# Performance work log

Measured on AMD Instinct MI355X. Metric: run time of the kernel, lower is better.

The kernel has to match this reference:

```python
import jax, jax.numpy as jnp
import numpy as np

C = 256
B, H, W = 2, 64, 64


def conv1x1(x, Wt, b):
    # x: [B, Cin, H, W], Wt: [Cout, Cin], b: [Cout]
    return jnp.einsum('bchw,oc->bohw', x, Wt) + b[None, :, None, None]


def setup_inputs() -> dict:
    key = jax.random.key(0)
    ks = jax.random.split(key, 16)
    s = 0.02
    d = {
        'input1': jax.random.normal(ks[0], (B, C, H, W), jnp.float32),
        'input2': jax.random.normal(ks[1], (B, C, H, W), jnp.float32),
        'Wq1': jax.random.normal(ks[2], (C // 4, C), jnp.float32) * s,
        'bq1': jnp.zeros((C // 4,), jnp.float32),
        'Wk1': jax.random.normal(ks[3], (C // 2, C), jnp.float32) * s,
        'bk1': jnp.zeros((C // 2,), jnp.float32),
        'Wv1': jax.random.normal(ks[4], (C, C), jnp.float32) * s,
        'bv1': jnp.zeros((C,), jnp.float32),
        'Wq2': jax.random.normal(ks[5], (C // 4, C), jnp.float32) * s,
        'bq2': jnp.zeros((C // 4,), jnp.float32),
        'Wk2': jax.random.normal(ks[6], (C // 2, C), jnp.float32) * s,
        'bk2': jnp.zeros((C // 2,), jnp.float32),
        'Wv2': jax.random.normal(ks[7], (C, C), jnp.float32) * s,
        'bv2': jnp.zeros((C,), jnp.float32),
        'gamma': jax.random.normal(ks[8], (1,), jnp.float32) * 0.1,
    }
    return d


def reference(input1, input2, Wq1, bq1, Wk1, bk1, Wv1, bv1,
              Wq2, bq2, Wk2, bk2, Wv2, bv2, gamma):
    b, c, h, w = input1.shape
    hw = h * w
    q1 = conv1x1(input1, Wq1, bq1)                      # [B, C/4, H, W]
    k1 = conv1x1(input1, Wk1, bk1).reshape(b, -1, hw)   # [B, C/2, HW]
    v1 = conv1x1(input1, Wv1, bv1).reshape(b, -1, hw)   # [B, C,   HW]
    q2 = conv1x1(input2, Wq2, bq2)
    k2 = conv1x1(input2, Wk2, bk2).reshape(b, -1, hw)
    v2 = conv1x1(input2, Wv2, bv2).reshape(b, -1, hw)

    # cat on new dim 2 then 'b c t h w -> b (c t) h w' interleaves q1/q2 channels
    q = jnp.stack([q1, q2], axis=2).reshape(b, c // 2, hw)  # [B, C/2, HW]
    q = q.transpose(0, 2, 1)                                # [B, HW, C/2]

    a1 = jax.nn.softmax(jnp.einsum('bnc,bcm->bnm', q, k1), axis=-1)  # [B, HW, HW]
    out1 = jnp.einsum('bcm,bnm->bcn', v1, a1).reshape(b, c, h, w)
    out1 = gamma[0] * out1 + input1

    a2 = jax.nn.softmax(jnp.einsum('bnc,bcm->bnm', q, k2), axis=-1)
    out2 = jnp.einsum('bcm,bnm->bcn', v2, a2).reshape(b, c, h, w)
    out2 = gamma[0] * out2 + input2
    return (out1, out2)
```

## Files before the change

kernel.cpp:

```cpp
#include <hip/hip_runtime.h>

typedef __attribute__((ext_vector_type(8)))  short bf16x8;
typedef __attribute__((ext_vector_type(4)))  float f32x4;
typedef __attribute__((ext_vector_type(16))) float f32x16;
typedef __attribute__((ext_vector_type(8)))  unsigned short u16x8;

#define HW 4096
#define CDIM 256

#if __has_builtin(__builtin_amdgcn_exp2f)
#define EXP2(x) __builtin_amdgcn_exp2f(x)
#else
#define EXP2(x) exp2f(x)
#endif

__device__ __forceinline__ unsigned short f2bf(float f) {
    union { float f; unsigned u; } v; v.f = f;
    unsigned r = v.u + 0x7fffu + ((v.u >> 16) & 1u);
    return (unsigned short)(r >> 16);
}
__device__ __forceinline__ float bf2f(unsigned short u) {
    union { unsigned u; float f; } v; v.u = ((unsigned)u) << 16;
    return v.f;
}
__device__ __forceinline__ unsigned pk2(float hi, float lo) {
    union { float f; unsigned u; } a, b; a.f = hi; b.f = lo;
    return __builtin_amdgcn_perm(a.u, b.u, 0x07060302u);
}
__device__ __forceinline__ void gl_lds16(const void* g, void* l) {
    __builtin_amdgcn_global_load_lds(
        (const __attribute__((address_space(1))) unsigned int*)(unsigned long long)g,
        (__attribute__((address_space(3))) unsigned int*)(unsigned int)(unsigned long long)l,
        16, 0, 0);
}

__global__ __launch_bounds__(256) void wpack_kernel(
    const float* __restrict__ Wq1, const float* __restrict__ Wk1,
    const float* __restrict__ Wv1, const float* __restrict__ Wq2,
    const float* __restrict__ Wk2, const float* __restrict__ Wv2,
    unsigned short* __restrict__ Wpk)
{
    const int i  = blockIdx.x * 256 + threadIdx.x;
    const int c4 = i & 63;
    const int r6 = i >> 6;
    const int inp = r6 / 448;
    const int o   = r6 - inp * 448;
    const float* src;
    int orow;
    if (o < 64)       { src = inp ? Wq2 : Wq1; orow = o; }
    else if (o < 192) { src = inp ? Wk2 : Wk1; orow = o - 64; }
    else              { src = inp ? Wv2 : Wv1; orow = o - 192; }
    const float4 v = *(const float4*)(src + (size_t)orow * CDIM + c4 * 4);
    uint2 pkd; pkd.x = pk2(v.y, v.x); pkd.y = pk2(v.w, v.z);
    ((uint2*)Wpk)[i] = pkd;
}

__global__ __launch_bounds__(256) void proj_kernel(
    const float* __restrict__ in1, const float* __restrict__ in2,
    const float* __restrict__ bq1, const float* __restrict__ bk1,
    const float* __restrict__ bv1, const float* __restrict__ bq2,
    const float* __restrict__ bk2, const float* __restrict__ bv2,
    const unsigned short* __restrict__ Wpk,
    unsigned short* __restrict__ Qg, unsigned short* __restrict__ Kg,
    unsigned short* __restrict__ Vg)
{
    __shared__ unsigned xb[32 * 128];

    const int bid   = blockIdx.x;
    const int ntile = bid & 127;
    const int inp   = (bid >> 7) & 1;
    const int b     = bid >> 8;

    const float* X  = (inp ? in2 : in1) + (size_t)b * CDIM * HW;
    const float* bq = inp ? bq2 : bq1;
    const float* bk = inp ? bk2 : bk1;
    const float* bv = inp ? bv2 : bv1;
    const unsigned short* Wb = Wpk + (size_t)inp * 448 * CDIM;

    const int tid  = threadIdx.x;
    const int lane = tid & 63;
    const int w    = tid >> 6;
    const int l15  = lane & 15, quad = lane >> 4;
    const int n0   = ntile * 32;

#pragma unroll
    for (int t = 0; t < 4; ++t) {
        const int idx = t * 256 + tid;
        const int cp  = idx >> 3;
        const int n4  = idx & 7;
        const float* p0 = X + (size_t)(cp * 2) * HW + n0 + n4 * 4;
        const float4 a = *(const float4*)p0;
        const float4 bb = *(const float4*)(p0 + HW);
        const float av[4] = {a.x, a.y, a.z, a.w};
        const float bv4[4] = {bb.x, bb.y, bb.z, bb.w};
#pragma unroll
        for (int r = 0; r < 4; ++r) {
            const int n = n4 * 4 + r;
            xb[n * 128 + (((cp >> 2) ^ (n & 7)) << 2) + (cp & 3)] = pk2(bv4[r], av[r]);
        }
    }
    __syncthreads();

    f32x4 acc[7][2];
#pragma unroll
    for (int i = 0; i < 7; ++i)
#pragma unroll
        for (int j = 0; j < 2; ++j) acc[i][j] = (f32x4){0.f, 0.f, 0.f, 0.f};

#pragma unroll
    for (int kk = 0; kk < 8; ++kk) {
        bf16x8 xf[2];
#pragma unroll
        for (int ns = 0; ns < 2; ++ns) {
            const int nrow = ns * 16 + l15;
            xf[ns] = *(const bf16x8*)&xb[nrow * 128 + (((kk * 4 + quad) ^ (nrow & 7)) << 2)];
        }
#pragma unroll
        for (int os = 0; os < 7; ++os) {
            const int ob = w * 7 + os;
            const int og = ob * 16 + l15;
            const bf16x8 wf = *(const bf16x8*)(Wb + (size_t)og * CDIM + kk * 32 + quad * 8);
            if (ob < 12) {
#pragma unroll
                for (int ns = 0; ns < 2; ++ns)
                    acc[os][ns] = __builtin_amdgcn_mfma_f32_16x16x32_bf16(xf[ns], wf, acc[os][ns], 0, 0, 0);
            } else {
#pragma unroll
                for (int ns = 0; ns < 2; ++ns)
                    acc[os][ns] = __builtin_amdgcn_mfma_f32_16x16x32_bf16(wf, xf[ns], acc[os][ns], 0, 0, 0);
            }
        }
    }

    const size_t qbase = (size_t)b * HW * 128;
    const size_t kbase = (size_t)(b * 2 + inp) * HW * 128;
    const size_t vbase = (size_t)(b * 2 + inp) * (size_t)CDIM * HW;
#pragma unroll
    for (int os = 0; os < 7; ++os) {
        const int ob = w * 7 + os;
        if (ob < 4) {
            const int o = ob * 16 + l15;
            const float bb = bq[o];
#pragma unroll
            for (int ns = 0; ns < 2; ++ns) {
                const f32x4 d = acc[os][ns];
#pragma unroll
                for (int r = 0; r < 4; ++r) {
                    const int n = n0 + ns * 16 + quad * 4 + r;
                    Qg[qbase + (size_t)n * 128 + 2 * o + inp] =
                        f2bf((d[r] + bb) * 1.4426950408889634f);
                }
            }
        } else if (ob < 12) {
            const int c = (ob - 4) * 16 + l15;
            const float bb = bk[c];
#pragma unroll
            for (int ns = 0; ns < 2; ++ns) {
                const f32x4 d = acc[os][ns];
#pragma unroll
                for (int r = 0; r < 4; ++r) {
                    const int n = n0 + ns * 16 + quad * 4 + r;
                    Kg[kbase + (size_t)n * 128 + c] = f2bf(d[r] + bb);
                }
            }
        } else {
            const int c0 = (ob - 12) * 16 + quad * 4;
#pragma unroll
            for (int ns = 0; ns < 2; ++ns) {
                const f32x4 d = acc[os][ns];
#pragma unroll
                for (int r = 0; r < 4; ++r) {
                    const int n = n0 + ns * 16 + l15;
                    Vg[vbase + (size_t)(c0 + r) * HW + n] = f2bf(d[r] + bv[c0 + r]);
                }
            }
        }
    }
}

__global__ __launch_bounds__(256, 2) void attn_kernel(
    const unsigned short* __restrict__ Qg, const unsigned short* __restrict__ Kg,
    const unsigned short* __restrict__ Vg,
    unsigned short* __restrict__ Op, float* __restrict__ Lp)
{
    __shared__ unsigned short kbuf[2][32 * 16 * 8];
    __shared__ unsigned short vbuf[3][256 * 4 * 8];

    const int bid = blockIdx.x;
    const int mq  = bid & 3;
    const int set = (bid >> 2) & 3;
    const int att = set & 1, b = set >> 1;
    const int nt  = bid >> 4;
    const int n0g = nt * 128;
    const int mbase = mq * 1024;
    const int tid = threadIdx.x;
    const int lane = tid & 63, w = tid >> 6;
    const int l31 = lane & 31, h = lane >> 5;

    const unsigned short* Qb = Qg + (size_t)b * HW * 128;
    const unsigned short* Kb = Kg + (size_t)(b * 2 + att) * HW * 128;
    const unsigned short* Vb = Vg + (size_t)(b * 2 + att) * (size_t)CDIM * HW;

    bf16x8 aQ[8];
    {
        const int n = n0g + w * 32 + l31;
#pragma unroll
        for (int kk = 0; kk < 8; ++kk)
            aQ[kk] = *(const bf16x8*)(Qb + (size_t)n * 128 + kk * 16 + h * 8);
    }

    f32x16 acc[8];
#pragma unroll
    for (int i = 0; i < 8; ++i)
#pragma unroll
        for (int r = 0; r < 16; ++r) acc[i][r] = 0.f;
    float lsum = 0.f;

    const unsigned short* ksrc[2];
    const unsigned short* vsrc[4];
#pragma unroll
    for (int t = 0; t < 2; ++t) {
        const int L = (t * 4 + w) * 64 + lane;
        const int ml = L >> 4, s = L & 15;
        ksrc[t] = Kb + (size_t)ml * 128 + (s ^ (ml & 15)) * 8;
    }
#pragma unroll
    for (int t = 0; t < 4; ++t) {
        const int L = (t * 4 + w) * 64 + lane;
        const int c = L >> 2, s = L & 3;
        vsrc[t] = Vb + (size_t)c * HW + (s ^ ((c >> 2) & 3)) * 8;
    }

    auto stage = [&](int mt) {
        const int kb = mt & 1;
        const int vb = mt % 3;
        const int m0 = mbase + mt * 32;
        char* kdl = (char*)&kbuf[kb][0] + (size_t)w * 1024;
        char* vdl = (char*)&vbuf[vb][0] + (size_t)w * 1024;
#pragma unroll
        for (int t = 0; t < 2; ++t)
            gl_lds16(ksrc[t] + (size_t)m0 * 128, kdl + (size_t)t * 4096);
#pragma unroll
        for (int t = 0; t < 4; ++t)
            gl_lds16(vsrc[t] + m0, vdl + (size_t)t * 4096);
    };

    auto QK = [&](const unsigned short* kb_, f32x16& sa, f32x16& sb) {
#pragma unroll
        for (int r = 0; r < 16; ++r) { sa[r] = 0.f; sb[r] = 0.f; }
#pragma unroll
        for (int kk = 0; kk < 4; ++kk) {
            bf16x8 bK = *(const bf16x8*)&kb_[(l31 * 16 + ((kk * 2 + h) ^ (l31 & 15))) * 8];
            sa = __builtin_amdgcn_mfma_f32_32x32x16_bf16(bK, aQ[kk], sa, 0, 0, 0);
        }
#pragma unroll
        for (int kk = 4; kk < 8; ++kk) {
            bf16x8 bK = *(const bf16x8*)&kb_[(l31 * 16 + ((kk * 2 + h) ^ (l31 & 15))) * 8];
            sb = __builtin_amdgcn_mfma_f32_32x32x16_bf16(bK, aQ[kk], sb, 0, 0, 0);
        }
    };

    auto EXPP = [&](const f32x16& sa, const f32x16& sb, bf16x8* bP) {
        float p[16];
#pragma unroll
        for (int r = 0; r < 16; ++r) {
            p[r] = EXP2(sa[r] + sb[r]);
            lsum += p[r];
        }
#pragma unroll
        for (int k2 = 0; k2 < 2; ++k2) {
            const float* pp = p + k2 * 8;
            const unsigned a0 = pk2(pp[1], pp[0]);
            const unsigned a1 = pk2(pp[3], pp[2]);
            const unsigned b0 = pk2(pp[5], pp[4]);
            const unsigned b1 = pk2(pp[7], pp[6]);
            auto s0 = __builtin_amdgcn_permlane32_swap(a0, b0, false, false);
            auto s1 = __builtin_amdgcn_permlane32_swap(a1, b1, false, false);
            union { unsigned u[4]; bf16x8 v; } uu;
            uu.u[0] = s0[0];
            uu.u[1] = s1[0];
            uu.u[2] = s0[1];
            uu.u[3] = s1[1];
            bP[k2] = uu.v;
        }
    };

    auto PV = [&](const unsigned short* vb_, const bf16x8* bP) {
#pragma unroll
        for (int cf = 0; cf < 8; ++cf) {
            const int c = cf * 32 + l31;
#pragma unroll
            for (int k2 = 0; k2 < 2; ++k2) {
                bf16x8 aV = *(const bf16x8*)&vb_[(c * 4 + ((k2 * 2 + h) ^ ((c >> 2) & 3))) * 8];
                acc[cf] = __builtin_amdgcn_mfma_f32_32x32x16_bf16(aV, bP[k2], acc[cf], 0, 0, 0);
            }
        }
    };

    stage(0);
    __syncthreads();
    stage(1);
    bf16x8 bP[2];
    {
        f32x16 sa, sb;
        QK(&kbuf[0][0], sa, sb);
        EXPP(sa, sb, bP);
    }
    int vprev = 0;
#pragma unroll 1
    for (int mt = 1; mt < 32; ++mt) {
        __syncthreads();
        if (mt + 1 < 32) stage(mt + 1);
        f32x16 sa, sb;
        QK(&kbuf[mt & 1][0], sa, sb);
        PV(&vbuf[vprev][0], bP);
        EXPP(sa, sb, bP);
        vprev = (vprev == 2) ? 0 : vprev + 1;
    }
    PV(&vbuf[vprev][0], bP);

    const float ltot = lsum + __shfl_xor(lsum, 32, 64);
    const int nn = n0g + w * 32 + l31;
    if (h == 0) Lp[(size_t)(mq * 4 + set) * HW + nn] = ltot;

    const size_t obase = (size_t)(mq * 4 + set) * CDIM * HW;
#pragma unroll
    for (int cf = 0; cf < 8; ++cf) {
#pragma unroll
        for (int r = 0; r < 16; ++r) {
            const int c = cf * 32 + (r & 3) + 8 * (r >> 2) + 4 * h;
            Op[obase + (size_t)c * HW + nn] = f2bf(acc[cf][r]);
        }
    }
}

__global__ __launch_bounds__(256) void combine_kernel(
    const unsigned short* __restrict__ Op, const float* __restrict__ Lp,
    const float* __restrict__ in1, const float* __restrict__ in2,
    const float* __restrict__ gamma_p, float* __restrict__ out)
{
    const size_t i8 = ((size_t)blockIdx.x * 256 + threadIdx.x) * 8;
    const int oset = (int)(i8 >> 20);
    const int att = oset >> 1, b = oset & 1;
    const int pset = b * 2 + att;
    const size_t rem = i8 & 1048575u;
    const int n = (int)(i8 & 4095);

    u16x8 o[4];
    f32x4 l0[4], l1[4];
#pragma unroll
    for (int mq = 0; mq < 4; ++mq) {
        o[mq]  = *(const u16x8*)(Op + ((size_t)(mq * 4 + pset) << 20) + rem);
        l0[mq] = *(const f32x4*)(Lp + (size_t)(mq * 4 + pset) * HW + n);
        l1[mq] = *(const f32x4*)(Lp + (size_t)(mq * 4 + pset) * HW + n + 4);
    }
    const float* inb = (att ? in2 : in1) + (size_t)b * CDIM * HW + rem;
    const float g = *gamma_p;

    const f32x4 iv0 = *(const f32x4*)(inb);
    const f32x4 iv1 = *(const f32x4*)(inb + 4);
    f32x4 r0, r1;
#pragma unroll
    for (int j = 0; j < 4; ++j) {
        float ov = 0.f, ld = 0.f;
#pragma unroll
        for (int mq = 0; mq < 4; ++mq) {
            ov += bf2f((unsigned short)o[mq][j]);
            ld += l0[mq][j];
        }
        r0[j] = g * ov / ld + iv0[j];
    }
#pragma unroll
    for (int j = 0; j < 4; ++j) {
        float ov = 0.f, ld = 0.f;
#pragma unroll
        for (int mq = 0; mq < 4; ++mq) {
            ov += bf2f((unsigned short)o[mq][j + 4]);
            ld += l1[mq][j];
        }
        r1[j] = g * ov / ld + iv1[j];
    }
    *(f32x4*)(out + i8) = r0;
    *(f32x4*)(out + i8 + 4) = r1;
}

extern "C" void kernel_launch(void* const* d_in, const int* in_sizes, int n_in,
                              void* d_out, int out_size, void* d_ws, size_t ws_size,
                              hipStream_t stream) {
    const float* in1 = (const float*)d_in[0];
    const float* in2 = (const float*)d_in[1];
    const float* Wq1 = (const float*)d_in[2];  const float* bq1 = (const float*)d_in[3];
    const float* Wk1 = (const float*)d_in[4];  const float* bk1 = (const float*)d_in[5];
    const float* Wv1 = (const float*)d_in[6];  const float* bv1 = (const float*)d_in[7];
    const float* Wq2 = (const float*)d_in[8];  const float* bq2 = (const float*)d_in[9];
    const float* Wk2 = (const float*)d_in[10]; const float* bk2 = (const float*)d_in[11];
    const float* Wv2 = (const float*)d_in[12]; const float* bv2 = (const float*)d_in[13];
    const float* gamma = (const float*)d_in[14];

    unsigned short* Qg = (unsigned short*)d_ws;
    unsigned short* Kg = Qg + (size_t)2 * HW * 128;
    unsigned short* Vg = Kg + (size_t)4 * HW * 128;
    unsigned short* Op = Vg + (size_t)4 * CDIM * HW;
    float*          Lp = (float*)(Op + (size_t)16 * CDIM * HW);
    unsigned short* Wpk = Op;

    wpack_kernel<<<224, 256, 0, stream>>>(Wq1, Wk1, Wv1, Wq2, Wk2, Wv2, Wpk);
    proj_kernel<<<512, 256, 0, stream>>>(in1, in2, bq1, bk1, bv1, bq2, bk2, bv2,
                                         Wpk, Qg, Kg, Vg);
    attn_kernel<<<512, 256, 0, stream>>>(Qg, Kg, Vg, Op, Lp);
    combine_kernel<<<2048, 256, 0, stream>>>(Op, Lp, in1, in2, gamma, (float*)d_out);
}
```

Before: 177.8 us.

## Use 8-wave attention blocks splitting keys in-block, halving partial outputs

The attention kernel now runs 512-thread blocks in which two groups of four waves each handle half of a 64-key tile. The two halves' partial outputs are reduced through shared memory before writing, so each block covers half the key range instead of a quarter. This halves the partial Op/Lp buffers and the combine kernel's reads, and the shared K/V staging tiles are larger. In exchange, the grid drops to 256 blocks, each needs 128KB of LDS and an extra reduction step with syncs, which may limit occupancy and latency hiding.

```diff
diff --git a/kernel.cpp b/kernel.cpp
--- a/kernel.cpp
+++ b/kernel.cpp
@@ -178,23 +178,27 @@
     }
 }
 
-__global__ __launch_bounds__(256, 2) void attn_kernel(
+__global__ __launch_bounds__(512, 2) void attn_kernel(
     const unsigned short* __restrict__ Qg, const unsigned short* __restrict__ Kg,
     const unsigned short* __restrict__ Vg,
     unsigned short* __restrict__ Op, float* __restrict__ Lp)
 {
-    __shared__ unsigned short kbuf[2][32 * 16 * 8];
-    __shared__ unsigned short vbuf[3][256 * 4 * 8];
+    __shared__ __align__(16) char smem[131072];
+    unsigned short* kbuf = (unsigned short*)smem;
+    unsigned short* vbuf = (unsigned short*)(smem + 32768);
+    unsigned*       ex32 = (unsigned*)smem;
+    float*          lred = (float*)(smem + 65536);
 
     const int bid = blockIdx.x;
-    const int mq  = bid & 3;
-    const int set = (bid >> 2) & 3;
+    const int mh  = bid & 1;
+    const int set = (bid >> 1) & 3;
     const int att = set & 1, b = set >> 1;
-    const int nt  = bid >> 4;
+    const int nt  = bid >> 3;
     const int n0g = nt * 128;
-    const int mbase = mq * 1024;
+    const int mbase = mh * 2048;
     const int tid = threadIdx.x;
     const int lane = tid & 63, w = tid >> 6;
+    const int nw = w & 3, mw = w >> 2;
     const int l31 = lane & 31, h = lane >> 5;
 
     const unsigned short* Qb = Qg + (size_t)b * HW * 128;
@@ -203,7 +207,7 @@
 
     bf16x8 aQ[8];
     {
-        const int n = n0g + w * 32 + l31;
+        const int n = n0g + nw * 32 + l31;
 #pragma unroll
         for (int kk = 0; kk < 8; ++kk)
             aQ[kk] = *(const bf16x8*)(Qb + (size_t)n * 128 + kk * 16 + h * 8);
@@ -220,32 +224,34 @@
     const unsigned short* vsrc[4];
 #pragma unroll
     for (int t = 0; t < 2; ++t) {
-        const int L = (t * 4 + w) * 64 + lane;
+        const int L = t * 512 + tid;
         const int ml = L >> 4, s = L & 15;
         ksrc[t] = Kb + (size_t)ml * 128 + (s ^ (ml & 15)) * 8;
     }
 #pragma unroll
     for (int t = 0; t < 4; ++t) {
-        const int L = (t * 4 + w) * 64 + lane;
-        const int c = L >> 2, s = L & 3;
-        vsrc[t] = Vb + (size_t)c * HW + (s ^ ((c >> 2) & 3)) * 8;
+        const int L = t * 512 + tid;
+        const int half = L >> 10, L1 = L & 1023;
+        const int c = L1 >> 2, s = L1 & 3;
+        vsrc[t] = Vb + (size_t)c * HW + half * 32 + (s ^ ((c >> 2) & 3)) * 8;
     }
 
     auto stage = [&](int mt) {
         const int kb = mt & 1;
         const int vb = mt % 3;
-        const int m0 = mbase + mt * 32;
-        char* kdl = (char*)&kbuf[kb][0] + (size_t)w * 1024;
-        char* vdl = (char*)&vbuf[vb][0] + (size_t)w * 1024;
+        const int m0 = mbase + mt * 64;
+        char* kdl = (char*)kbuf + (size_t)kb * 16384 + (size_t)w * 1024;
+        char* vdl = (char*)vbuf + (size_t)vb * 32768 + (size_t)w * 1024;
 #pragma unroll
         for (int t = 0; t < 2; ++t)
-            gl_lds16(ksrc[t] + (size_t)m0 * 128, kdl + (size_t)t * 4096);
+            gl_lds16(ksrc[t] + (size_t)m0 * 128, kdl + (size_t)t * 8192);
 #pragma unroll
         for (int t = 0; t < 4; ++t)
-            gl_lds16(vsrc[t] + m0, vdl + (size_t)t * 4096);
+            gl_lds16(vsrc[t] + m0, vdl + (size_t)t * 8192);
     };
 
-    auto QK = [&](const unsigned short* kb_, f32x16& sa, f32x16& sb) {
+    auto QK = [&](int cur, f32x16& sa, f32x16& sb) {
+        const unsigned short* kb_ = kbuf + cur * 8192 + mw * 4096;
 #pragma unroll
         for (int r = 0; r < 16; ++r) { sa[r] = 0.f; sb[r] = 0.f; }
 #pragma unroll
@@ -285,7 +291,8 @@
         }
     };
 
-    auto PV = [&](const unsigned short* vb_, const bf16x8* bP) {
+    auto PV = [&](int vprev, const bf16x8* bP) {
+        const unsigned short* vb_ = vbuf + vprev * 16384 + mw * 8192;
 #pragma unroll
         for (int cf = 0; cf < 8; ++cf) {
             const int c = cf * 32 + l31;
@@ -303,7 +310,7 @@
     bf16x8 bP[2];
     {
         f32x16 sa, sb;
-        QK(&kbuf[0][0], sa, sb);
+        QK(0, sa, sb);
         EXPP(sa, sb, bP);
     }
     int vprev = 0;
@@ -312,24 +319,48 @@
         __syncthreads();
         if (mt + 1 < 32) stage(mt + 1);
         f32x16 sa, sb;
-        QK(&kbuf[mt & 1][0], sa, sb);
-        PV(&vbuf[vprev][0], bP);
+        QK(mt & 1, sa, sb);
+        PV(vprev, bP);
         EXPP(sa, sb, bP);
         vprev = (vprev == 2) ? 0 : vprev + 1;
     }
-    PV(&vbuf[vprev][0], bP);
-
-    const float ltot = lsum + __shfl_xor(lsum, 32, 64);
-    const int nn = n0g + w * 32 + l31;
-    if (h == 0) Lp[(size_t)(mq * 4 + set) * HW + nn] = ltot;
-
-    const size_t obase = (size_t)(mq * 4 + set) * CDIM * HW;
-#pragma unroll
-    for (int cf = 0; cf < 8; ++cf) {
-#pragma unroll
-        for (int r = 0; r < 16; ++r) {
-            const int c = cf * 32 + (r & 3) + 8 * (r >> 2) + 4 * h;
-            Op[obase + (size_t)c * HW + nn] = f2bf(acc[cf][r]);
+    PV(vprev, bP);
+
+    const float lw = lsum + __shfl_xor(lsum, 32, 64);
+    __syncthreads();
+    if (h == 0) lred[w * 32 + l31] = lw;
+    if (mw == 1) {
+#pragma unroll
+        for (int cf = 0; cf < 8; ++cf)
+#pragma unroll
+            for (int rp = 0; rp < 8; ++rp) {
+                const unsigned v = ((unsigned)f2bf(acc[cf][rp * 2 + 1]) << 16)
+                                 | f2bf(acc[cf][rp * 2]);
+                ex32[(((w - 4) * 8 + cf) * 8 + rp) * 64 + lane] = v;
+            }
+    }
+    __syncthreads();
+    if (mw == 0) {
+#pragma unroll
+        for (int cf = 0; cf < 8; ++cf)
+#pragma unroll
+            for (int rp = 0; rp < 8; ++rp) {
+                const unsigned v = ex32[((w * 8 + cf) * 8 + rp) * 64 + lane];
+                acc[cf][rp * 2]     += bf2f((unsigned short)(v & 0xffffu));
+                acc[cf][rp * 2 + 1] += bf2f((unsigned short)(v >> 16));
+            }
+        const float ltot = lred[w * 32 + l31] + lred[(w + 4) * 32 + l31];
+        const int nn = n0g + nw * 32 + l31;
+        if (h == 0) Lp[(size_t)(mh * 4 + set) * HW + nn] = ltot;
+
+        const size_t obase = (size_t)(mh * 4 + set) * CDIM * HW;
+#pragma unroll
+        for (int cf = 0; cf < 8; ++cf) {
+#pragma unroll
+            for (int r = 0; r < 16; ++r) {
+                const int c = cf * 32 + (r & 3) + 8 * (r >> 2) + 4 * h;
+                Op[obase + (size_t)c * HW + nn] = f2bf(acc[cf][r]);
+            }
         }
     }
 }
@@ -346,14 +377,12 @@
     const size_t rem = i8 & 1048575u;
     const int n = (int)(i8 & 4095);
 
-    u16x8 o[4];
-    f32x4 l0[4], l1[4];
-#pragma unroll
-    for (int mq = 0; mq < 4; ++mq) {
-        o[mq]  = *(const u16x8*)(Op + ((size_t)(mq * 4 + pset) << 20) + rem);
-        l0[mq] = *(const f32x4*)(Lp + (size_t)(mq * 4 + pset) * HW + n);
-        l1[mq] = *(const f32x4*)(Lp + (size_t)(mq * 4 + pset) * HW + n + 4);
-    }
+    const u16x8 o0 = *(const u16x8*)(Op + ((size_t)pset << 20) + rem);
+    const u16x8 o1 = *(const u16x8*)(Op + ((size_t)pset << 20) + rem + ((size_t)4 << 20));
+    const f32x4 la0 = *(const f32x4*)(Lp + (size_t)pset * HW + n);
+    const f32x4 la1 = *(const f32x4*)(Lp + (size_t)pset * HW + n + 4);
+    const f32x4 lb0 = *(const f32x4*)(Lp + (size_t)(4 + pset) * HW + n);
+    const f32x4 lb1 = *(const f32x4*)(Lp + (size_t)(4 + pset) * HW + n + 4);
     const float* inb = (att ? in2 : in1) + (size_t)b * CDIM * HW + rem;
     const float g = *gamma_p;
 
@@ -362,23 +391,13 @@
     f32x4 r0, r1;
 #pragma unroll
     for (int j = 0; j < 4; ++j) {
-        float ov = 0.f, ld = 0.f;
-#pragma unroll
-        for (int mq = 0; mq < 4; ++mq) {
-            ov += bf2f((unsigned short)o[mq][j]);
-            ld += l0[mq][j];
-        }
-        r0[j] = g * ov / ld + iv0[j];
+        const float ov = bf2f((unsigned short)o0[j]) + bf2f((unsigned short)o1[j]);
+        r0[j] = g * ov / (la0[j] + lb0[j]) + iv0[j];
     }
 #pragma unroll
     for (int j = 0; j < 4; ++j) {
-        float ov = 0.f, ld = 0.f;
-#pragma unroll
-        for (int mq = 0; mq < 4; ++mq) {
-            ov += bf2f((unsigned short)o[mq][j + 4]);
-            ld += l1[mq][j];
-        }
-        r1[j] = g * ov / ld + iv1[j];
+        const float ov = bf2f((unsigned short)o0[j + 4]) + bf2f((unsigned short)o1[j + 4]);
+        r1[j] = g * ov / (la1[j] + lb1[j]) + iv1[j];
     }
     *(f32x4*)(out + i8) = r0;
     *(f32x4*)(out + i8 + 4) = r1;
@@ -401,12 +420,12 @@
     unsigned short* Kg = Qg + (size_t)2 * HW * 128;
     unsigned short* Vg = Kg + (size_t)4 * HW * 128;
     unsigned short* Op = Vg + (size_t)4 * CDIM * HW;
-    float*          Lp = (float*)(Op + (size_t)16 * CDIM * HW);
+    float*          Lp = (float*)(Op + (size_t)8 * CDIM * HW);
     unsigned short* Wpk = Op;
 
     wpack_kernel<<<224, 256, 0, stream>>>(Wq1, Wk1, Wv1, Wq2, Wk2, Wv2, Wpk);
     proj_kernel<<<512, 256, 0, stream>>>(in1, in2, bq1, bk1, bv1, bq2, bk2, bv2,
                                          Wpk, Qg, Kg, Vg);
-    attn_kernel<<<512, 256, 0, stream>>>(Qg, Kg, Vg, Op, Lp);
+    attn_kernel<<<256, 512, 0, stream>>>(Qg, Kg, Vg, Op, Lp);
     combine_kernel<<<2048, 256, 0, stream>>>(Op, Lp, in1, in2, gamma, (float*)d_out);
 }
```

Result: no change. 177.2 us (-0.4%).
